# Performance work log

Hardware: AMD Instinct MI355X
Metric: run time of the kernel (lower is better)

Reference implementation:

```python
import jax, jax.numpy as jnp
import numpy as np

B, N, C_IN = 32, 1024, 128
F0, F1, F2 = 64, 64, 64
OUT = 10
RATIOS = (0.8, 0.8)
EPS = 1e-5


def setup_inputs() -> dict:
    key = jax.random.key(0)
    ks = jax.random.split(key, 16)
    N_nodes = jax.random.randint(ks[0], (B,), N // 2, N + 1)
    mask = (jnp.arange(N)[None, :] < N_nodes[:, None]).astype(jnp.float32)
    x = jax.random.normal(ks[1], (B, N, C_IN), dtype=jnp.float32)
    # sparse-ish symmetric binary adjacency restricted to valid nodes
    A = (jax.random.uniform(ks[2], (B, N, N)) < 0.02).astype(jnp.float32)
    A = jnp.maximum(A, jnp.swapaxes(A, 1, 2))
    A = A * mask[:, :, None] * mask[:, None, :]
    def lin(k, fi, fo):
        b = 1.0 / np.sqrt(fi)
        kw, kb = jax.random.split(k)
        return (jax.random.uniform(kw, (fi, fo), minval=-b, maxval=b),
                jax.random.uniform(kb, (fo,), minval=-b, maxval=b))
    W0, b0 = lin(ks[3], C_IN, F0)
    W1, b1 = lin(ks[4], F0, F1)
    W2, b2 = lin(ks[5], F1, F2)
    bp0 = 1.0 / np.sqrt(F0)
    p0 = jax.random.uniform(ks[6], (F0, 1), minval=-bp0, maxval=bp0)
    bp1 = 1.0 / np.sqrt(F1)
    p1 = jax.random.uniform(ks[7], (F1, 1), minval=-bp1, maxval=bp1)
    Wfc, bfc = lin(ks[8], F2, OUT)
    return {"x": x, "A": A, "mask": mask, "N_nodes": N_nodes,
            "W0": W0, "b0": b0, "W1": W1, "b1": b1, "W2": W2, "b2": b2,
            "p0": p0, "p1": p1, "Wfc": Wfc, "bfc": bfc}


def _gconv(x, A, W, b):
    # Kipf-Welling normalized Laplacian conv, batched dense
    n = A.shape[1]
    A_hat = A + jnp.eye(n, dtype=A.dtype)[None]
    D = (jnp.sum(A_hat, axis=1) + EPS) ** -0.5  # [B,N]
    L = D[:, :, None] * A_hat * D[:, None, :]
    h = jnp.einsum('bnm,bmc->bnc', L, x) @ W + b
    return jax.nn.relu(h)


def _pool(x, A, mask, N_nodes, p, ratio):
    Bc, Nc, C = x.shape
    y = (x.reshape(Bc * Nc, C) @ p).reshape(Bc, Nc)
    y = y / jnp.sqrt(jnp.sum(p ** 2))
    N_remove = (N_nodes.astype(jnp.float32) * (1.0 - ratio)).astype(N_nodes.dtype)
    # remove the N_remove lowest-scoring valid nodes per graph
    y_eff = jnp.where(mask > 0, y, jnp.inf)
    ranks = jnp.argsort(jnp.argsort(y_eff, axis=1), axis=1)  # ascending rank
    new_mask = mask * (ranks >= N_remove[:, None]).astype(mask.dtype)
    x = x * jnp.tanh(y)[:, :, None] * new_mask[:, :, None]
    A = new_mask[:, :, None] * A * new_mask[:, None, :]
    return x, A, new_mask, N_nodes - N_remove


def reference(x, A, mask, N_nodes, W0, b0, W1, b1, W2, b2, p0, p1, Wfc, bfc):
    x = _gconv(x, A, W0, b0)
    x, A, mask, N_nodes = _pool(x, A, mask, N_nodes, p0, RATIOS[0])
    x = _gconv(x, A, W1, b1)
    x, A, mask, N_nodes = _pool(x, A, mask, N_nodes, p1, RATIOS[1])
    x = _gconv(x, A, W2, b2)
    x = jnp.max(x, axis=1)  # global max pool over nodes [B,F2]
    return x @ Wfc + bfc
```

## Files before the change

### kernel.cpp

```cpp
#include <hip/hip_runtime.h>
#include <cstdint>
#include <cstddef>

#define BB 32
#define NN 1024
#define CIN 128
#define FF 64
#define NOUT 10
#define CAP 128
#define EPSV 1e-5f

__global__ __launch_bounds__(256) void k_front(const float* __restrict__ A,
                                               const float* __restrict__ x,
                                               const float* __restrict__ W0,
                                               unsigned short* __restrict__ adj,
                                               int* __restrict__ cnt,
                                               float* __restrict__ c1,
                                               float* __restrict__ c2,
                                               float* __restrict__ T) {
    __shared__ __align__(16) float Wl[64 * 64];
    int tid = threadIdx.x;
    int wave = tid >> 6, lane = tid & 63;
    if (blockIdx.x >= 8192) {
        int gid = blockIdx.x - 8192;
        int b = gid & 31;
        int cch = gid >> 5;
        int row0 = (b << 10) + cch * 16;
        int rsub = lane >> 4, f0 = (lane & 15) * 4;
        int r = row0 + wave * 4 + rsub;
        const float4* xr = (const float4*)(x + (size_t)r * CIN);
        float4 acc = {0.f, 0.f, 0.f, 0.f};
#pragma unroll
        for (int kc = 0; kc < 2; ++kc) {
            if (kc) __syncthreads();
            for (int t = tid; t < 64 * 16; t += 256)
                ((float4*)Wl)[t] = ((const float4*)W0)[kc * 1024 + t];
            __syncthreads();
#pragma unroll 4
            for (int k4 = 0; k4 < 16; ++k4) {
                float4 xv = xr[kc * 16 + k4];
                float4 w0 = *(const float4*)&Wl[(k4 * 4 + 0) * 64 + f0];
                float4 w1 = *(const float4*)&Wl[(k4 * 4 + 1) * 64 + f0];
                float4 w2 = *(const float4*)&Wl[(k4 * 4 + 2) * 64 + f0];
                float4 w3 = *(const float4*)&Wl[(k4 * 4 + 3) * 64 + f0];
                acc.x += xv.x * w0.x; acc.y += xv.x * w0.y; acc.z += xv.x * w0.z; acc.w += xv.x * w0.w;
                acc.x += xv.y * w1.x; acc.y += xv.y * w1.y; acc.z += xv.y * w1.z; acc.w += xv.y * w1.w;
                acc.x += xv.z * w2.x; acc.y += xv.z * w2.y; acc.z += xv.z * w2.z; acc.w += xv.z * w2.w;
                acc.x += xv.w * w3.x; acc.y += xv.w * w3.y; acc.z += xv.w * w3.z; acc.w += xv.w * w3.w;
            }
        }
        *(float4*)&T[(size_t)r * 64 + f0] = acc;
    } else {
        unsigned short* adjs = ((unsigned short*)Wl) + wave * CAP;
        int r = blockIdx.x * 4 + wave;
        const float4* Arow = (const float4*)(A + (size_t)r * NN);
        float4 v0 = Arow[lane];
        float4 v1 = Arow[64 + lane];
        float4 v2 = Arow[128 + lane];
        float4 v3 = Arow[192 + lane];
        int c = 0;
        unsigned long long lt = (lane == 0) ? 0ULL : ((1ULL << lane) - 1ULL);
        float4 vv[4] = {v0, v1, v2, v3};
#pragma unroll
        for (int it = 0; it < 4; ++it) {
            float4 v = vv[it];
            int j0 = it * 256 + lane * 4;
            unsigned long long m0 = __ballot(v.x != 0.f);
            unsigned long long m1 = __ballot(v.y != 0.f);
            unsigned long long m2 = __ballot(v.z != 0.f);
            unsigned long long m3 = __ballot(v.w != 0.f);
            int before = __popcll(m0 & lt) + __popcll(m1 & lt) +
                         __popcll(m2 & lt) + __popcll(m3 & lt);
            int p = c + before;
            if (v.x != 0.f) { if (p < CAP) adjs[p] = (unsigned short)(j0 + 0); ++p; }
            if (v.y != 0.f) { if (p < CAP) adjs[p] = (unsigned short)(j0 + 1); ++p; }
            if (v.z != 0.f) { if (p < CAP) adjs[p] = (unsigned short)(j0 + 2); ++p; }
            if (v.w != 0.f) { if (p < CAP) adjs[p] = (unsigned short)(j0 + 3); ++p; }
            c += __popcll(m0) + __popcll(m1) + __popcll(m2) + __popcll(m3);
        }
        int cc = (c > CAP) ? CAP : c;
        uint32_t* dst = (uint32_t*)(adj + (size_t)r * CAP);
        if (lane * 2 < cc) dst[lane] = ((const uint32_t*)adjs)[lane];
        if (lane == 0) {
            cnt[r] = cc;
            float D = 1.0f / sqrtf((float)c + 1.0f + EPSV);
            c1[r] = D;
            c2[r] = D * D;
        }
    }
}

__global__ __launch_bounds__(256) void k_mid(const unsigned short* __restrict__ adj,
                                             const int* __restrict__ cnt,
                                             const float* __restrict__ nm,
                                             float* __restrict__ c1, float* __restrict__ c2,
                                             const float* __restrict__ Xin,
                                             const float* __restrict__ W,
                                             const float* __restrict__ y,
                                             float* __restrict__ T) {
    __shared__ __align__(16) float Wl[64 * 64];
    int tid = threadIdx.x;
    if (blockIdx.x >= 8192) {
        int gid = blockIdx.x - 8192;
        int b = gid & 31;
        int cch = gid >> 5;
        int row0 = (b << 10) + cch * 16;
        for (int t = tid; t < 64 * 16; t += 256)
            ((float4*)Wl)[t] = ((const float4*)W)[t];
        __syncthreads();
        int wave = tid >> 6, lane = tid & 63;
        int rsub = lane >> 4, f0 = (lane & 15) * 4;
        int r = row0 + wave * 4 + rsub;
        float sc = tanhf(y[r]) * nm[r];
        const float4* xr = (const float4*)(Xin + (size_t)r * 64);
        float4 acc = {0.f, 0.f, 0.f, 0.f};
#pragma unroll 4
        for (int k4 = 0; k4 < 16; ++k4) {
            float4 xv = xr[k4];
            float4 w0 = *(const float4*)&Wl[(k4 * 4 + 0) * 64 + f0];
            float4 w1 = *(const float4*)&Wl[(k4 * 4 + 1) * 64 + f0];
            float4 w2 = *(const float4*)&Wl[(k4 * 4 + 2) * 64 + f0];
            float4 w3 = *(const float4*)&Wl[(k4 * 4 + 3) * 64 + f0];
            acc.x += xv.x * w0.x; acc.y += xv.x * w0.y; acc.z += xv.x * w0.z; acc.w += xv.x * w0.w;
            acc.x += xv.y * w1.x; acc.y += xv.y * w1.y; acc.z += xv.y * w1.z; acc.w += xv.y * w1.w;
            acc.x += xv.z * w2.x; acc.y += xv.z * w2.y; acc.z += xv.z * w2.z; acc.w += xv.z * w2.w;
            acc.x += xv.w * w3.x; acc.y += xv.w * w3.y; acc.z += xv.w * w3.z; acc.w += xv.w * w3.w;
        }
        acc.x *= sc; acc.y *= sc; acc.z *= sc; acc.w *= sc;
        *(float4*)&T[(size_t)r * 64 + f0] = acc;
    } else {
        int wave = tid >> 6, lane = tid & 63;
        int r = blockIdx.x * 4 + wave;
        int b = r >> 10;
        const unsigned short* arow = adj + (size_t)r * CAP;
        const float* nmb = nm + (b << 10);
        int n = cnt[r];
        float s = 0.f;
        if (lane < n)      s  = nmb[arow[lane]];
        if (lane + 64 < n) s += nmb[arow[lane + 64]];
        for (int sh = 32; sh; sh >>= 1) s += __shfl_xor(s, sh, 64);
        if (lane == 0) {
            float m = nm[r];
            float D = 1.0f / sqrtf(m * s + 1.0f + EPSV);
            c1[r] = m * D;
            c2[r] = D * D;
        }
    }
}

__global__ __launch_bounds__(256) void k_spmm(const unsigned short* __restrict__ adj,
                                              const int* __restrict__ cnt,
                                              const float* __restrict__ c1,
                                              const float* __restrict__ c2,
                                              const float* __restrict__ T,
                                              const float* __restrict__ bias,
                                              float* __restrict__ X,
                                              const float* __restrict__ p,
                                              float* __restrict__ y,
                                              float* __restrict__ gmax) {
    __shared__ __align__(16) float c1s[NN];
    __shared__ float red[4][64];
    int b   = blockIdx.x & 31;
    int cch = blockIdx.x >> 5;
    int tid = threadIdx.x;
    ((float4*)c1s)[tid] = ((const float4*)(c1 + (b << 10)))[tid];
    __syncthreads();
    int wave = tid >> 6, lane = tid & 63;
    int r0 = (b << 10) + cch * 16 + wave * 4;
    const float* Tb = T + ((size_t)(b << 10) << 6);
    float bv = bias[lane];
    float pv = 0.f, ppinv = 0.f;
    if (p != nullptr) {
        pv = p[lane];
        float pp = pv * pv;
        for (int s = 32; s; s >>= 1) pp += __shfl_xor(pp, s, 64);
        ppinv = 1.0f / sqrtf(pp);
    }
    float vmax = 0.f;
#pragma unroll
    for (int rr = 0; rr < 4; ++rr) {
        int r = r0 + rr;
        const unsigned short* arow = adj + (size_t)r * CAP;
        int n = cnt[r];
        float acc0 = 0.f, acc1 = 0.f, acc2 = 0.f, acc3 = 0.f;
        int t = 0;
        for (; t + 4 <= n; t += 4) {
            ushort4 j4 = *(const ushort4*)(arow + t);
            acc0 += c1s[j4.x] * Tb[((int)j4.x << 6) + lane];
            acc1 += c1s[j4.y] * Tb[((int)j4.y << 6) + lane];
            acc2 += c1s[j4.z] * Tb[((int)j4.z << 6) + lane];
            acc3 += c1s[j4.w] * Tb[((int)j4.w << 6) + lane];
        }
        for (; t < n; ++t) {
            int j = arow[t];
            acc0 += c1s[j] * Tb[(j << 6) + lane];
        }
        float acc = (acc0 + acc1) + (acc2 + acc3);
        int rl = r & 1023;
        float o = c1s[rl] * acc + c2[r] * T[((size_t)r << 6) + lane] + bv;
        o = fmaxf(o, 0.f);
        if (X != nullptr) X[((size_t)r << 6) + lane] = o;
        if (p != nullptr) {
            float a = o * pv;
            for (int s = 32; s; s >>= 1) a += __shfl_xor(a, s, 64);
            if (lane == 0) y[r] = a * ppinv;
        }
        vmax = fmaxf(vmax, o);
    }
    if (gmax != nullptr) {
        red[wave][lane] = vmax;
        __syncthreads();
        if (wave == 0) {
            float m = fmaxf(fmaxf(red[0][lane], red[1][lane]),
                            fmaxf(red[2][lane], red[3][lane]));
            atomicMax((int*)&gmax[(b << 6) + lane], __float_as_int(m));
        }
    }
}

__global__ __launch_bounds__(256) void k_rank(const float* __restrict__ y,
                                              const float* __restrict__ maskSrc,
                                              const int* __restrict__ nsrc,
                                              float* __restrict__ nmOut,
                                              int* __restrict__ ncur) {
    __shared__ __align__(16) float yv[NN];
    int b = blockIdx.x >> 4;
    int sub = blockIdx.x & 15;
    int tid = threadIdx.x;
    const float INF = __builtin_inff();
    {
        float4 v = ((const float4*)(y + (b << 10)))[tid];
        float4 m = ((const float4*)(maskSrc + (b << 10)))[tid];
        v.x = (m.x > 0.f) ? v.x : INF;
        v.y = (m.y > 0.f) ? v.y : INF;
        v.z = (m.z > 0.f) ? v.z : INF;
        v.w = (m.w > 0.f) ? v.w : INF;
        ((float4*)yv)[tid] = v;
    }
    int n = nsrc[b];
    const float RM = (float)(1.0 - 0.8);
    int nrem = (int)((float)n * RM);
    if (sub == 0 && tid == 0) ncur[b] = n - nrem;
    __syncthreads();
    int i = (sub << 6) + (tid >> 2);
    int q = tid & 3;
    float yi = yv[i];
    int rank = 0;
    if (yi < INF) {
        const float4* jbase = (const float4*)yv + (q << 6);
        int j0 = q << 8;
#pragma unroll 8
        for (int t = 0; t < 64; ++t) {
            float4 a = jbase[t];
            int j = j0 + t * 4;
            rank += (a.x < yi || (a.x == yi && j     < i)) ? 1 : 0;
            rank += (a.y < yi || (a.y == yi && j + 1 < i)) ? 1 : 0;
            rank += (a.z < yi || (a.z == yi && j + 2 < i)) ? 1 : 0;
            rank += (a.w < yi || (a.w == yi && j + 3 < i)) ? 1 : 0;
        }
    }
    rank += __shfl_xor(rank, 1, 64);
    rank += __shfl_xor(rank, 2, 64);
    if (q == 0) {
        float nmv = (yi < INF && rank >= nrem) ? 1.f : 0.f;
        nmOut[(b << 10) + i] = nmv;
    }
}

__global__ __launch_bounds__(64) void k_fc(const float* __restrict__ gmax,
                                           const float* __restrict__ Wfc,
                                           const float* __restrict__ bfc,
                                           float* __restrict__ out) {
    __shared__ float gl[64];
    int b = blockIdx.x, lane = threadIdx.x;
    gl[lane] = gmax[(b << 6) + lane];
    __syncthreads();
    if (lane < NOUT) {
        float acc = bfc[lane];
        for (int k = 0; k < 64; ++k) acc += gl[k] * Wfc[k * NOUT + lane];
        out[b * NOUT + lane] = acc;
    }
}

extern "C" void kernel_launch(void* const* d_in, const int* in_sizes, int n_in,
                              void* d_out, int out_size, void* d_ws, size_t ws_size,
                              hipStream_t stream) {
    const float* x    = (const float*)d_in[0];
    const float* A    = (const float*)d_in[1];
    const float* mask = (const float*)d_in[2];
    const int*   Nn   = (const int*)d_in[3];
    const float* W0   = (const float*)d_in[4];
    const float* b0   = (const float*)d_in[5];
    const float* W1   = (const float*)d_in[6];
    const float* b1   = (const float*)d_in[7];
    const float* W2   = (const float*)d_in[8];
    const float* b2   = (const float*)d_in[9];
    const float* p0   = (const float*)d_in[10];
    const float* p1   = (const float*)d_in[11];
    const float* Wfc  = (const float*)d_in[12];
    const float* bfc  = (const float*)d_in[13];
    float* out = (float*)d_out;

    char* ws = (char*)d_ws;
    size_t off = 0;
    auto alloc = [&](size_t bytes) -> void* {
        void* p = ws + off;
        off = (off + bytes + 255) & ~(size_t)255;
        return p;
    };
    unsigned short* adj = (unsigned short*)alloc((size_t)BB * NN * CAP * 2);
    int*   cnt  = (int*)  alloc((size_t)BB * NN * 4);
    float* X    = (float*)alloc((size_t)BB * NN * 64 * 4);
    float* T    = (float*)alloc((size_t)BB * NN * 64 * 4);
    float* c1   = (float*)alloc((size_t)BB * NN * 4);
    float* c2   = (float*)alloc((size_t)BB * NN * 4);
    float* y    = (float*)alloc((size_t)BB * NN * 4);
    float* nm0  = (float*)alloc((size_t)BB * NN * 4);
    float* nm1  = (float*)alloc((size_t)BB * NN * 4);
    int*   nc0  = (int*)  alloc((size_t)BB * 4);
    int*   nc1  = (int*)  alloc((size_t)BB * 4);
    float* gmax = (float*)alloc((size_t)BB * 64 * 4);

    hipMemsetAsync(gmax, 0, (size_t)BB * 64 * 4, stream);
    k_front<<<8192 + 2048, 256, 0, stream>>>(A, x, W0, adj, cnt, c1, c2, T);
    k_spmm<<<2048, 256, 0, stream>>>(adj, cnt, c1, c2, T, b0, X, p0, y, nullptr);
    k_rank<<<BB * 16, 256, 0, stream>>>(y, mask, Nn, nm0, nc0);
    k_mid<<<8192 + 2048, 256, 0, stream>>>(adj, cnt, nm0, c1, c2, X, W1, y, T);
    k_spmm<<<2048, 256, 0, stream>>>(adj, cnt, c1, c2, T, b1, X, p1, y, nullptr);
    k_rank<<<BB * 16, 256, 0, stream>>>(y, nm0, nc0, nm1, nc1);
    k_mid<<<8192 + 2048, 256, 0, stream>>>(adj, cnt, nm1, c1, c2, X, W2, y, T);
    k_spmm<<<2048, 256, 0, stream>>>(adj, cnt, c1, c2, T, b2, nullptr, nullptr, nullptr, gmax);
    k_fc<<<BB, 64, 0, stream>>>(gmax, Wfc, bfc, out);
}
```

Before: 374.2 us.

## Skip rows and columns beyond each graph's valid node count across all kernels

Uses the per-graph node count N_nodes to skip work on padded rows in the adjacency compaction, feature transforms, SpMM and ranking kernels. It also limits A-row loads and rank comparisons to the valid prefix. The gmax memset is replaced by an extra k_front block that initialises gmax to relu(b2), which accounts for padded nodes that are no longer processed. Correctness depends on mask being a prefix of length N_nodes and on skipped rows never being read downstream.

```diff
diff --git a/kernel.cpp b/kernel.cpp
--- a/kernel.cpp
+++ b/kernel.cpp
@@ -13,6 +13,9 @@
 __global__ __launch_bounds__(256) void k_front(const float* __restrict__ A,
                                                const float* __restrict__ x,
                                                const float* __restrict__ W0,
+                                               const int* __restrict__ Nn,
+                                               const float* __restrict__ b2f,
+                                               float* __restrict__ gmax,
                                                unsigned short* __restrict__ adj,
                                                int* __restrict__ cnt,
                                                float* __restrict__ c1,
@@ -21,10 +24,16 @@
     __shared__ __align__(16) float Wl[64 * 64];
     int tid = threadIdx.x;
     int wave = tid >> 6, lane = tid & 63;
+    if (blockIdx.x >= 10240) {
+        for (int i = tid; i < BB * 64; i += 256)
+            gmax[i] = fmaxf(b2f[i & 63], 0.f);
+        return;
+    }
     if (blockIdx.x >= 8192) {
         int gid = blockIdx.x - 8192;
         int b = gid & 31;
         int cch = gid >> 5;
+        if (cch * 16 >= Nn[b]) return;
         int row0 = (b << 10) + cch * 16;
         int rsub = lane >> 4, f0 = (lane & 15) * 4;
         int r = row0 + wave * 4 + rsub;
@@ -51,13 +60,27 @@
         }
         *(float4*)&T[(size_t)r * 64 + f0] = acc;
     } else {
+        int r = blockIdx.x * 4 + wave;
+        int b = r >> 10;
+        int Nb = Nn[b];
+        int rl = r & 1023;
+        if (rl >= Nb) {
+            if (lane == 0) {
+                cnt[r] = 0;
+                float D = 1.0f / sqrtf(1.0f + EPSV);
+                c1[r] = D;
+                c2[r] = D * D;
+            }
+            return;
+        }
         unsigned short* adjs = ((unsigned short*)Wl) + wave * CAP;
-        int r = blockIdx.x * 4 + wave;
         const float4* Arow = (const float4*)(A + (size_t)r * NN);
+        int nch = (Nb + 255) >> 8;
+        float4 z4 = {0.f, 0.f, 0.f, 0.f};
         float4 v0 = Arow[lane];
         float4 v1 = Arow[64 + lane];
-        float4 v2 = Arow[128 + lane];
-        float4 v3 = Arow[192 + lane];
+        float4 v2 = (nch > 2) ? Arow[128 + lane] : z4;
+        float4 v3 = (nch > 3) ? Arow[192 + lane] : z4;
         int c = 0;
         unsigned long long lt = (lane == 0) ? 0ULL : ((1ULL << lane) - 1ULL);
         float4 vv[4] = {v0, v1, v2, v3};
@@ -97,13 +120,15 @@
                                              const float* __restrict__ Xin,
                                              const float* __restrict__ W,
                                              const float* __restrict__ y,
-                                             float* __restrict__ T) {
+                                             float* __restrict__ T,
+                                             const int* __restrict__ Nn) {
     __shared__ __align__(16) float Wl[64 * 64];
     int tid = threadIdx.x;
     if (blockIdx.x >= 8192) {
         int gid = blockIdx.x - 8192;
         int b = gid & 31;
         int cch = gid >> 5;
+        if (cch * 16 >= Nn[b]) return;
         int row0 = (b << 10) + cch * 16;
         for (int t = tid; t < 64 * 16; t += 256)
             ((float4*)Wl)[t] = ((const float4*)W)[t];
@@ -132,6 +157,7 @@
         int wave = tid >> 6, lane = tid & 63;
         int r = blockIdx.x * 4 + wave;
         int b = r >> 10;
+        if ((r & 1023) >= Nn[b]) return;
         const unsigned short* arow = adj + (size_t)r * CAP;
         const float* nmb = nm + (b << 10);
         int n = cnt[r];
@@ -157,13 +183,17 @@
                                               float* __restrict__ X,
                                               const float* __restrict__ p,
                                               float* __restrict__ y,
-                                              float* __restrict__ gmax) {
+                                              float* __restrict__ gmax,
+                                              const int* __restrict__ Nn) {
     __shared__ __align__(16) float c1s[NN];
     __shared__ float red[4][64];
     int b   = blockIdx.x & 31;
     int cch = blockIdx.x >> 5;
+    int Nb = Nn[b];
+    if (cch * 16 >= Nb) return;
     int tid = threadIdx.x;
-    ((float4*)c1s)[tid] = ((const float4*)(c1 + (b << 10)))[tid];
+    int n4 = (Nb + 3) >> 2;
+    if (tid < n4) ((float4*)c1s)[tid] = ((const float4*)(c1 + (b << 10)))[tid];
     __syncthreads();
     int wave = tid >> 6, lane = tid & 63;
     int r0 = (b << 10) + cch * 16 + wave * 4;
@@ -180,6 +210,8 @@
 #pragma unroll
     for (int rr = 0; rr < 4; ++rr) {
         int r = r0 + rr;
+        int rl = r & 1023;
+        if (rl >= Nb) break;
         const unsigned short* arow = adj + (size_t)r * CAP;
         int n = cnt[r];
         float acc0 = 0.f, acc1 = 0.f, acc2 = 0.f, acc3 = 0.f;
@@ -196,7 +228,6 @@
             acc0 += c1s[j] * Tb[(j << 6) + lane];
         }
         float acc = (acc0 + acc1) + (acc2 + acc3);
-        int rl = r & 1023;
         float o = c1s[rl] * acc + c2[r] * T[((size_t)r << 6) + lane] + bv;
         o = fmaxf(o, 0.f);
         if (X != nullptr) X[((size_t)r << 6) + lane] = o;
@@ -221,6 +252,7 @@
 __global__ __launch_bounds__(256) void k_rank(const float* __restrict__ y,
                                               const float* __restrict__ maskSrc,
                                               const int* __restrict__ nsrc,
+                                              const int* __restrict__ nbound,
                                               float* __restrict__ nmOut,
                                               int* __restrict__ ncur) {
     __shared__ __align__(16) float yv[NN];
@@ -228,13 +260,19 @@
     int sub = blockIdx.x & 15;
     int tid = threadIdx.x;
     const float INF = __builtin_inff();
+    int Nb = nbound[b];
     {
-        float4 v = ((const float4*)(y + (b << 10)))[tid];
-        float4 m = ((const float4*)(maskSrc + (b << 10)))[tid];
-        v.x = (m.x > 0.f) ? v.x : INF;
-        v.y = (m.y > 0.f) ? v.y : INF;
-        v.z = (m.z > 0.f) ? v.z : INF;
-        v.w = (m.w > 0.f) ? v.w : INF;
+        float4 v;
+        if (tid * 4 < Nb) {
+            v = ((const float4*)(y + (b << 10)))[tid];
+            float4 m = ((const float4*)(maskSrc + (b << 10)))[tid];
+            v.x = (m.x > 0.f) ? v.x : INF;
+            v.y = (m.y > 0.f) ? v.y : INF;
+            v.z = (m.z > 0.f) ? v.z : INF;
+            v.w = (m.w > 0.f) ? v.w : INF;
+        } else {
+            v.x = INF; v.y = INF; v.z = INF; v.w = INF;
+        }
         ((float4*)yv)[tid] = v;
     }
     int n = nsrc[b];
@@ -249,8 +287,10 @@
     if (yi < INF) {
         const float4* jbase = (const float4*)yv + (q << 6);
         int j0 = q << 8;
+        int tend = (Nb - j0 + 3) >> 2;
+        if (tend > 64) tend = 64;
 #pragma unroll 8
-        for (int t = 0; t < 64; ++t) {
+        for (int t = 0; t < tend; ++t) {
             float4 a = jbase[t];
             int j = j0 + t * 4;
             rank += (a.x < yi || (a.x == yi && j     < i)) ? 1 : 0;
@@ -321,14 +361,15 @@
     int*   nc1  = (int*)  alloc((size_t)BB * 4);
     float* gmax = (float*)alloc((size_t)BB * 64 * 4);
 
-    hipMemsetAsync(gmax, 0, (size_t)BB * 64 * 4, stream);
-    k_front<<<8192 + 2048, 256, 0, stream>>>(A, x, W0, adj, cnt, c1, c2, T);
-    k_spmm<<<2048, 256, 0, stream>>>(adj, cnt, c1, c2, T, b0, X, p0, y, nullptr);
-    k_rank<<<BB * 16, 256, 0, stream>>>(y, mask, Nn, nm0, nc0);
-    k_mid<<<8192 + 2048, 256, 0, stream>>>(adj, cnt, nm0, c1, c2, X, W1, y, T);
-    k_spmm<<<2048, 256, 0, stream>>>(adj, cnt, c1, c2, T, b1, X, p1, y, nullptr);
-    k_rank<<<BB * 16, 256, 0, stream>>>(y, nm0, nc0, nm1, nc1);
-    k_mid<<<8192 + 2048, 256, 0, stream>>>(adj, cnt, nm1, c1, c2, X, W2, y, T);
-    k_spmm<<<2048, 256, 0, stream>>>(adj, cnt, c1, c2, T, b2, nullptr, nullptr, nullptr, gmax);
+    k_front<<<8192 + 2048 + 1, 256, 0, stream>>>(A, x, W0, Nn, b2, gmax,
+                                                 adj, cnt, c1, c2, T);
+    k_spmm<<<2048, 256, 0, stream>>>(adj, cnt, c1, c2, T, b0, X, p0, y, nullptr, Nn);
+    k_rank<<<BB * 16, 256, 0, stream>>>(y, mask, Nn, Nn, nm0, nc0);
+    k_mid<<<8192 + 2048, 256, 0, stream>>>(adj, cnt, nm0, c1, c2, X, W1, y, T, Nn);
+    k_spmm<<<2048, 256, 0, stream>>>(adj, cnt, c1, c2, T, b1, X, p1, y, nullptr, Nn);
+    k_rank<<<BB * 16, 256, 0, stream>>>(y, nm0, nc0, Nn, nm1, nc1);
+    k_mid<<<8192 + 2048, 256, 0, stream>>>(adj, cnt, nm1, c1, c2, X, W2, y, T, Nn);
+    k_spmm<<<2048, 256, 0, stream>>>(adj, cnt, c1, c2, T, b2, nullptr, nullptr, nullptr,
+                                     gmax, Nn);
     k_fc<<<BB, 64, 0, stream>>>(gmax, Wfc, bfc, out);
 }
```

Result: faster. 362.8 us (-3.0%).
